# Kernel optimization log

Hardware: AMD Instinct MI355X
Metric: run time of the kernel (lower is better)

The kernel has to match this reference:

```python
import jax, jax.numpy as jnp
import numpy as np

T, B, H, NH = 1024, 4, 1024, 16
D = H // NH


def setup_inputs() -> dict:
    key = jax.random.key(0)
    ks = jax.random.split(key, 8)
    s = 0.02
    return {
        "x": jax.random.normal(ks[0], (T, B, H), jnp.float32),
        "pos": jax.random.normal(ks[1], (2 * T - 1, 1, H), jnp.float32),
        "attn_mask": jnp.zeros((T, T), jnp.bool_),
        "ln_w": jnp.ones((H,), jnp.float32),
        "ln_b": jnp.zeros((H,), jnp.float32),
        "in_proj_w": jax.random.normal(ks[2], (3 * H, H), jnp.float32) * s,
        "in_proj_b": jnp.zeros((3 * H,), jnp.float32),
        "pos_proj_w": jax.random.normal(ks[3], (H, H), jnp.float32) * s,
        "r_w_bias": jax.random.normal(ks[4], (NH, D), jnp.float32) * s,
        "r_r_bias": jax.random.normal(ks[5], (NH, D), jnp.float32) * s,
        "out_proj_w": jax.random.normal(ks[6], (H, H), jnp.float32) * s,
        "out_proj_b": jnp.zeros((H,), jnp.float32),
    }


def _layer_norm(x, w, b, eps=1e-5):
    m = jnp.mean(x, axis=-1, keepdims=True)
    v = jnp.var(x, axis=-1, keepdims=True)
    return (x - m) * jax.lax.rsqrt(v + eps) * w + b


def _rel_shift(x):
    # x: [qlen, 2*qlen-1, B, NH] -> Transformer-XL relative shift
    q = x.shape[0]
    zero_pad = jnp.zeros((q, 1) + x.shape[2:], x.dtype)
    xp = jnp.concatenate([zero_pad, x], axis=1)            # [q, 2q, B, NH]
    xp = xp.reshape((x.shape[1] + 1, q) + x.shape[2:])     # [2q, q, B, NH]
    return xp[1:].reshape(x.shape)                         # [q, 2q-1, B, NH]


def reference(x, pos, attn_mask, ln_w, ln_b, in_proj_w, in_proj_b,
              pos_proj_w, r_w_bias, r_r_bias, out_proj_w, out_proj_b):
    # pre-norm
    qn = _layer_norm(x, ln_w, ln_b)                        # [T,B,H]
    # fused qkv projection
    qkv = qn @ in_proj_w.T + in_proj_b                     # [T,B,3H]
    q, k, v = jnp.split(qkv, 3, axis=-1)
    q = q.reshape(T, B, NH, D)
    k = k.reshape(T, B, NH, D)
    v = v.reshape(T, B, NH, D)
    # relative position keys (bias-free projection)
    r = (pos[:, 0] @ pos_proj_w.T).reshape(2 * T - 1, NH, D)
    # content term (AC) and position term (BD), Transformer-XL style
    AC = jnp.einsum('ibnd,jbnd->ijbn', q + r_w_bias, k)    # [T,T,B,NH]
    BD = jnp.einsum('ibnd,jnd->ijbn', q + r_r_bias, r)     # [T,2T-1,B,NH]
    BD = _rel_shift(BD)[:, :T]                             # [T,T,B,NH]
    scale = 1.0 / np.sqrt(D).astype(np.float32)
    score = (AC + BD) * scale
    score = jnp.where(attn_mask[:, :, None, None], -jnp.inf, score)
    p = jax.nn.softmax(score, axis=1)                      # coverage
    out = jnp.einsum('ijbn,jbnd->ibnd', p, v).reshape(T, B, H)
    o = out @ out_proj_w.T + out_proj_b                    # residual dropout = identity (eval)
    return o
```

## Files before the change

### kernel.cpp

```cpp
#include <hip/hip_runtime.h>
#include <hip/hip_bf16.h>
#include <math.h>

#define T_DIM 1024
#define B_DIM 4
#define H_DIM 1024
#define NHEAD 16
#define DHEAD 64
#define NROWS (T_DIM * B_DIM)
#define LPOS  (2 * T_DIM - 1)
#define QS    (3 * H_DIM)

typedef __attribute__((ext_vector_type(8))) short bfrag;
typedef __attribute__((ext_vector_type(4))) short sh4;
typedef __attribute__((ext_vector_type(4))) float facc;

static __device__ __forceinline__ short f2bf(float f) {
    return __builtin_bit_cast(short, __float2bfloat16(f));
}
static __device__ __forceinline__ float bf2f(short s) {
    unsigned u = ((unsigned)(unsigned short)s) << 16;
    return __builtin_bit_cast(float, u);
}

#define GLD16(g, l) __builtin_amdgcn_global_load_lds( \
    (const __attribute__((address_space(1))) void*)(g), \
    (__attribute__((address_space(3))) void*)(l), 16, 0, 0)

__global__ __launch_bounds__(256) void prep_kernel(
    const float* __restrict__ x, const float* __restrict__ lnw,
    const float* __restrict__ lnb, short* __restrict__ qn,
    const float* __restrict__ s0, short* __restrict__ d0, int c0,
    const float* __restrict__ s1, short* __restrict__ d1, int c1,
    const float* __restrict__ s2, short* __restrict__ d2, int c2,
    const float* __restrict__ s3, short* __restrict__ d3, int c3) {
    __shared__ float red0[4], red1[4];
    const int bid = blockIdx.x;
    const int tid = threadIdx.x;
    if (bid < NROWS) {
        const float* xr = x + (size_t)bid * H_DIM;
        short* yr = qn + (size_t)bid * H_DIM;
        float4 v = reinterpret_cast<const float4*>(xr)[tid];
        float s  = v.x + v.y + v.z + v.w;
        float sq = v.x * v.x + v.y * v.y + v.z * v.z + v.w * v.w;
        #pragma unroll
        for (int m = 32; m; m >>= 1) {
            s  += __shfl_xor(s, m);
            sq += __shfl_xor(sq, m);
        }
        int wave = tid >> 6, lane = tid & 63;
        if (lane == 0) { red0[wave] = s; red1[wave] = sq; }
        __syncthreads();
        float tot   = red0[0] + red0[1] + red0[2] + red0[3];
        float totsq = red1[0] + red1[1] + red1[2] + red1[3];
        float mean = tot * (1.0f / H_DIM);
        float var  = totsq * (1.0f / H_DIM) - mean * mean;
        float rstd = rsqrtf(var + 1e-5f);
        float4 wv = reinterpret_cast<const float4*>(lnw)[tid];
        float4 bv = reinterpret_cast<const float4*>(lnb)[tid];
        sh4 o;
        o[0] = f2bf((v.x - mean) * rstd * wv.x + bv.x);
        o[1] = f2bf((v.y - mean) * rstd * wv.y + bv.y);
        o[2] = f2bf((v.z - mean) * rstd * wv.z + bv.z);
        o[3] = f2bf((v.w - mean) * rstd * wv.w + bv.w);
        reinterpret_cast<sh4*>(yr)[tid] = o;
    } else {
        int i = (bid - NROWS) * 256 + tid;
        const float* s; short* d; int off;
        if      (i < c0)                { s = s0; d = d0; off = i; }
        else if (i < c0 + c1)           { s = s1; d = d1; off = i - c0; }
        else if (i < c0 + c1 + c2)      { s = s2; d = d2; off = i - c0 - c1; }
        else if (i < c0 + c1 + c2 + c3) { s = s3; d = d3; off = i - c0 - c1 - c2; }
        else return;
        const float* sp = s + (size_t)off * 8;
        float4 a = *(const float4*)(sp);
        float4 b = *(const float4*)(sp + 4);
        bfrag f;
        f[0] = f2bf(a.x); f[1] = f2bf(a.y); f[2] = f2bf(a.z); f[3] = f2bf(a.w);
        f[4] = f2bf(b.x); f[5] = f2bf(b.y); f[6] = f2bf(b.z); f[7] = f2bf(b.w);
        *(bfrag*)(d + (size_t)off * 8) = f;
    }
}

template<int MODE>
static __device__ __forceinline__ void gemm_body(
    const short* __restrict__ A, const short* __restrict__ B,
    const float* __restrict__ bias, void* __restrict__ Cv,
    int M, int N, int K, int gx, int nblk, int bid,
    short (*As)[64], short (*Bs)[64]) {
    const int tid = threadIdx.x;
    const int w4 = tid >> 6, l = tid & 63;
    const int lc = l & 15, lg = l >> 4;
    const int wr = w4 >> 1, wc = w4 & 1;

    const int cpx = nblk >> 3;
    const int nl = (bid & 7) * cpx + (bid >> 3);
    const int row0 = (nl / gx) * 128, col0 = (nl % gx) * 128;

    const int srow = l >> 3;
    const int schunk = ((l & 7) ^ srow) * 8;
    const int Mm1 = M - 1;

    facc acc[4][4];
    #pragma unroll
    for (int i = 0; i < 4; ++i)
        #pragma unroll
        for (int j = 0; j < 4; ++j) acc[i][j] = (facc){0.f, 0.f, 0.f, 0.f};

    for (int k0 = 0; k0 < K; k0 += 64) {
        #pragma unroll
        for (int p = 0; p < 4; ++p) {
            int rA = p * 32 + w4 * 8 + srow;
            int ga = row0 + rA; if (ga > Mm1) ga = Mm1;
            GLD16(A + (size_t)ga * K + k0 + schunk,
                  (char*)As + p * 4096 + w4 * 1024);
            GLD16(B + (size_t)(col0 + rA) * K + k0 + schunk,
                  (char*)Bs + p * 4096 + w4 * 1024);
        }
        __syncthreads();

        bfrag af[4][2], bfr[4][2];
        #pragma unroll
        for (int fr = 0; fr < 4; ++fr) {
            const int ra = wr * 64 + fr * 16 + lc;
            #pragma unroll
            for (int ks = 0; ks < 2; ++ks)
                af[fr][ks] = *(const bfrag*)&As[ra][(((ks * 4 + lg) ^ (ra & 7)) << 3)];
        }
        #pragma unroll
        for (int fc = 0; fc < 4; ++fc) {
            const int rb = wc * 64 + fc * 16 + lc;
            #pragma unroll
            for (int ks = 0; ks < 2; ++ks)
                bfr[fc][ks] = *(const bfrag*)&Bs[rb][(((ks * 4 + lg) ^ (rb & 7)) << 3)];
        }
        #pragma unroll
        for (int fr = 0; fr < 4; ++fr)
            #pragma unroll
            for (int fc = 0; fc < 4; ++fc)
                #pragma unroll
                for (int ks = 0; ks < 2; ++ks)
                    acc[fr][fc] = __builtin_amdgcn_mfma_f32_16x16x32_bf16(
                        af[fr][ks], bfr[fc][ks], acc[fr][fc], 0, 0, 0);
        __syncthreads();
    }

    #pragma unroll
    for (int fc = 0; fc < 4; ++fc) {
        const int gc = col0 + wc * 64 + fc * 16 + lc;
        const float bv = bias ? bias[gc] : 0.f;
        #pragma unroll
        for (int fr = 0; fr < 4; ++fr) {
            #pragma unroll
            for (int rg = 0; rg < 4; ++rg) {
                const int gr = row0 + wr * 64 + fr * 16 + lg * 4 + rg;
                if (gr < M) {
                    float o = acc[fr][fc][rg] + bv;
                    if constexpr (MODE == 0) ((float*)Cv)[(size_t)gr * N + gc] = o;
                    else                     ((short*)Cv)[(size_t)gr * N + gc] = f2bf(o);
                }
            }
        }
    }
}

__global__ __launch_bounds__(256) void gemm_dual(
    const short* __restrict__ A0, const short* __restrict__ B0,
    const float* __restrict__ bias0, short* __restrict__ C0,
    const short* __restrict__ A1, const short* __restrict__ B1,
    short* __restrict__ C1) {
    __shared__ short As[128][64];
    __shared__ short Bs[128][64];
    const int bid = blockIdx.x;
    if (bid < 768)
        gemm_body<1>(A0, B0, bias0, C0, NROWS, QS, H_DIM, QS / 128, 768, bid, As, Bs);
    else
        gemm_body<1>(A1, B1, nullptr, C1, LPOS, H_DIM, H_DIM, H_DIM / 128, 128, bid - 768, As, Bs);
}

__global__ __launch_bounds__(256) void gemm_f32out(
    const short* __restrict__ A, const short* __restrict__ B,
    const float* __restrict__ bias, float* __restrict__ C) {
    __shared__ short As[128][64];
    __shared__ short Bs[128][64];
    gemm_body<0>(A, B, bias, C, NROWS, H_DIM, H_DIM, H_DIM / 128, 256, blockIdx.x, As, Bs);
}

__global__ __launch_bounds__(256) void vtrans_kernel(const short* __restrict__ qkv,
                                                     short* __restrict__ vT) {
    __shared__ short T[64][72];
    const int tt = blockIdx.x, hh = blockIdx.y, b = blockIdx.z;
    const int tid = threadIdx.x;
    const int w = tid >> 6, lane = tid & 63;

    const int tg = tt * 64 + lane;
    const short* src = qkv + (size_t)(tg * B_DIM + b) * QS + 2 * H_DIM + hh * 64 + w * 16;
    bfrag v0 = *(const bfrag*)(src);
    bfrag v1 = *(const bfrag*)(src + 8);
    #pragma unroll
    for (int e = 0; e < 8; ++e) T[w * 16 + e][lane] = v0[e];
    #pragma unroll
    for (int e = 0; e < 8; ++e) T[w * 16 + 8 + e][lane] = v1[e];
    __syncthreads();

    const int hd = tid >> 2, tc = tid & 3;
    bfrag o0 = *(const bfrag*)&T[hd][tc * 16];
    bfrag o1 = *(const bfrag*)&T[hd][tc * 16 + 8];
    short* dst = vT + (((size_t)(b * H_DIM + hh * 64 + hd)) << 10) + tt * 64 + tc * 16;
    *(bfrag*)(dst) = o0;
    *(bfrag*)(dst + 8) = o1;
}

__global__ __launch_bounds__(256) void attn_mfma(const short* __restrict__ qkv,
                                                 const short* __restrict__ r,
                                                 const short* __restrict__ vt,
                                                 const float* __restrict__ rwb,
                                                 const float* __restrict__ rrb,
                                                 short* __restrict__ out) {
    __shared__ short Ks[64][64];
    __shared__ short Vt[64][64];
    __shared__ short Rs[128][64];
    __shared__ short BDs[4][16][84];
    __shared__ short Ps[4][16][76];

    const int d_   = blockIdx.y * 16 + blockIdx.x;
    const int slot = d_ >> 3, xcd = d_ & 7;
    const int bn   = xcd + 8 * (slot >> 4);
    const int i0   = (slot & 15) * 64;
    const int b    = bn >> 4;
    const int n    = bn & 15;

    const int tid = threadIdx.x;
    const int w   = tid >> 6;
    const int l   = tid & 63;
    const int lg  = l >> 4;
    const int lc  = l & 15;
    const int hoff = n * DHEAD;

    const int srow8 = l >> 3;
    const int sc8   = ((l & 7) ^ srow8) * 8;

    bfrag qw[2], qr[2];
    {
        const int row = i0 + 16 * w + lc;
        const short* qrow = qkv + (size_t)(row * B_DIM + b) * QS + hoff;
        #pragma unroll
        for (int ks = 0; ks < 2; ++ks) {
            const int d0 = ks * 32 + lg * 8;
            bfrag qv = *(const bfrag*)(qrow + d0);
            float4 wa = *(const float4*)(rwb + hoff + d0);
            float4 wb = *(const float4*)(rwb + hoff + d0 + 4);
            float4 ra = *(const float4*)(rrb + hoff + d0);
            float4 rb = *(const float4*)(rrb + hoff + d0 + 4);
            const float sc = 0.125f * 1.44269504f;
            float wf[8] = {wa.x, wa.y, wa.z, wa.w, wb.x, wb.y, wb.z, wb.w};
            float rf[8] = {ra.x, ra.y, ra.z, ra.w, rb.x, rb.y, rb.z, rb.w};
            bfrag fw, fr;
            #pragma unroll
            for (int e = 0; e < 8; ++e) {
                float qf = bf2f(qv[e]);
                fw[e] = f2bf((qf + wf[e]) * sc);
                fr[e] = f2bf((qf + rf[e]) * sc);
            }
            qw[ks] = fw; qr[ks] = fr;
        }
    }

    facc ofr[4];
    #pragma unroll
    for (int d = 0; d < 4; ++d) ofr[d] = (facc){0.f, 0.f, 0.f, 0.f};
    float lrow[4] = {0.f, 0.f, 0.f, 0.f};
    const int wbase = 16 * (3 - w);

    const short* kp0 = qkv + ((size_t)((w * 2 + 0) * 8 + srow8) * B_DIM + b) * QS + H_DIM + hoff + sc8;
    const short* kp1 = qkv + ((size_t)((w * 2 + 1) * 8 + srow8) * B_DIM + b) * QS + H_DIM + hoff + sc8;
    const short* vp0 = vt + (((size_t)(b * H_DIM + hoff + (w * 2 + 0) * 8 + srow8)) << 10) + sc8;
    const short* vp1 = vt + (((size_t)(b * H_DIM + hoff + (w * 2 + 1) * 8 + srow8)) << 10) + sc8;
    const size_t kstep = (size_t)64 * B_DIM * QS;
    char* const ksd0 = (char*)Ks + (w * 2 + 0) * 1024;
    char* const ksd1 = (char*)Ks + (w * 2 + 1) * 1024;
    char* const vtd0 = (char*)Vt + (w * 2 + 0) * 1024;
    char* const vtd1 = (char*)Vt + (w * 2 + 1) * 1024;

    for (int jt = 0; jt < 16; ++jt) {
        const int l_min = jt * 64 + 960 - i0;

        GLD16(kp0, ksd0);
        GLD16(kp1, ksd1);
        #pragma unroll
        for (int p = 0; p < 4; ++p) {
            const int c16 = w * 4 + p;
            int lrw = l_min + c16 * 8 + srow8; if (lrw > 2046) lrw = 2046;
            GLD16(r + (size_t)lrw * H_DIM + hoff + sc8,
                  (char*)Rs + c16 * 1024);
        }
        GLD16(vp0, vtd0);
        GLD16(vp1, vtd1);
        kp0 += kstep; kp1 += kstep; vp0 += 64; vp1 += 64;
        __syncthreads();

        __builtin_amdgcn_s_setprio(1);
        facc sfr[4];
        #pragma unroll
        for (int js = 0; js < 4; ++js) {
            sfr[js] = (facc){-4.f, -4.f, -4.f, -4.f};
            const int jrow = js * 16 + lc;
            #pragma unroll
            for (int ks = 0; ks < 2; ++ks) {
                const int ch = (ks * 4 + lg) ^ (jrow & 7);
                bfrag bf = *(const bfrag*)&Ks[jrow][ch << 3];
                sfr[js] = __builtin_amdgcn_mfma_f32_16x16x32_bf16(qw[ks], bf, sfr[js], 0, 0, 0);
            }
        }
        #pragma unroll
        for (int ls = 0; ls < 5; ++ls) {
            facc bd = (facc){-4.f, -4.f, -4.f, -4.f};
            const int rrow = wbase + ls * 16 + lc;
            #pragma unroll
            for (int ks = 0; ks < 2; ++ks) {
                const int ch = (ks * 4 + lg) ^ (rrow & 7);
                bfrag bf = *(const bfrag*)&Rs[rrow][ch << 3];
                bd = __builtin_amdgcn_mfma_f32_16x16x32_bf16(qr[ks], bf, bd, 0, 0, 0);
            }
            #pragma unroll
            for (int rg = 0; rg < 4; ++rg)
                BDs[w][lg * 4 + rg][ls * 16 + lc] = f2bf(bd[rg]);
        }
        __builtin_amdgcn_s_setprio(0);

        #pragma unroll
        for (int js = 0; js < 4; ++js)
            #pragma unroll
            for (int rg = 0; rg < 4; ++rg) {
                const int irow = lg * 4 + rg;
                float v = sfr[js][rg] + bf2f(BDs[w][irow][js * 16 + lc - irow + 15]);
                float p = exp2f(v);
                lrow[rg] += p;
                Ps[w][irow][js * 16 + lc] = f2bf(p);
            }

        bfrag pf[2];
        #pragma unroll
        for (int ks = 0; ks < 2; ++ks)
            pf[ks] = *(const bfrag*)&Ps[w][lc][ks * 32 + lg * 8];
        __builtin_amdgcn_s_setprio(1);
        #pragma unroll
        for (int d = 0; d < 4; ++d) {
            #pragma unroll
            for (int ks = 0; ks < 2; ++ks) {
                const int vr = d * 16 + lc;
                const int ch = (ks * 4 + lg) ^ (vr & 7);
                bfrag vf = *(const bfrag*)&Vt[vr][ch << 3];
                ofr[d] = __builtin_amdgcn_mfma_f32_16x16x32_bf16(pf[ks], vf, ofr[d], 0, 0, 0);
            }
        }
        __builtin_amdgcn_s_setprio(0);
        __syncthreads();
    }

    #pragma unroll
    for (int m = 1; m < 16; m <<= 1)
        #pragma unroll
        for (int rg = 0; rg < 4; ++rg)
            lrow[rg] += __shfl_xor(lrow[rg], m);

    #pragma unroll
    for (int rg = 0; rg < 4; ++rg) {
        const float inv = 1.0f / lrow[rg];
        const int row = i0 + 16 * w + lg * 4 + rg;
        short* orow = out + (size_t)(row * B_DIM + b) * H_DIM + hoff;
        #pragma unroll
        for (int d = 0; d < 4; ++d)
            orow[d * 16 + lc] = f2bf(ofr[d][rg] * inv);
    }
}

extern "C" void kernel_launch(void* const* d_in, const int* in_sizes, int n_in,
                              void* d_out, int out_size, void* d_ws, size_t ws_size,
                              hipStream_t stream) {
    const float* x          = (const float*)d_in[0];
    const float* pos        = (const float*)d_in[1];
    const float* ln_w       = (const float*)d_in[3];
    const float* ln_b       = (const float*)d_in[4];
    const float* in_proj_w  = (const float*)d_in[5];
    const float* in_proj_b  = (const float*)d_in[6];
    const float* pos_proj_w = (const float*)d_in[7];
    const float* r_w_bias   = (const float*)d_in[8];
    const float* r_r_bias   = (const float*)d_in[9];
    const float* out_proj_w = (const float*)d_in[10];
    const float* out_proj_b = (const float*)d_in[11];
    float* out = (float*)d_out;

    short* qn   = (short*)d_ws;
    short* qkv  = qn + (size_t)NROWS * H_DIM;
    short* rbuf = qkv + (size_t)NROWS * QS;
    short* wi   = rbuf + (size_t)2048 * H_DIM;
    short* wp   = wi + (size_t)QS * H_DIM;
    short* wo   = wp + (size_t)H_DIM * H_DIM;
    short* posb = wo + (size_t)H_DIM * H_DIM;
    short* vT   = posb + (size_t)2048 * H_DIM;

    const int c0 = (LPOS * H_DIM) / 8;
    const int c1 = (QS * H_DIM) / 8;
    const int c2 = (H_DIM * H_DIM) / 8;
    const int c3 = c2;
    const int nchunk = c0 + c1 + c2 + c3;
    const int cvtblk = (nchunk + 255) / 256;
    prep_kernel<<<NROWS + cvtblk, 256, 0, stream>>>(
        x, ln_w, ln_b, qn,
        pos, posb, c0, in_proj_w, wi, c1, pos_proj_w, wp, c2, out_proj_w, wo, c3);

    gemm_dual<<<768 + 128, 256, 0, stream>>>(qn, wi, in_proj_b, qkv, posb, wp, rbuf);

    vtrans_kernel<<<dim3(16, 16, 4), 256, 0, stream>>>(qkv, vT);

    attn_mfma<<<dim3(T_DIM / 64, B_DIM * NHEAD), 256, 0, stream>>>(
        qkv, rbuf, vT, r_w_bias, r_r_bias, qn);

    gemm_f32out<<<256, 256, 0, stream>>>(qn, wo, out_proj_b, out);
}
```

Baseline: 184.2 us.

## Prefetch next K/V/R tiles into registers to overlap global loads with compute

Replaces the direct global-to-LDS loads at the top of each key-tile iteration with register staging. The next tile's K, V and R fragments are loaded into registers while the current tile's MFMAs run, then written to LDS after a barrier. The goal is to hide global memory latency behind the score and PV computation. In exchange it costs extra VGPRs for the staging buffers and adds a second barrier per iteration, which may hurt occupancy.

New measurement: 175.5 us. 4.7% less time.

```diff
diff --git a/kernel.cpp b/kernel.cpp
--- a/kernel.cpp
+++ b/kernel.cpp
@@ -277,27 +277,40 @@
     const short* vp0 = vt + (((size_t)(b * H_DIM + hoff + (w * 2 + 0) * 8 + srow8)) << 10) + sc8;
     const short* vp1 = vt + (((size_t)(b * H_DIM + hoff + (w * 2 + 1) * 8 + srow8)) << 10) + sc8;
     const size_t kstep = (size_t)64 * B_DIM * QS;
-    char* const ksd0 = (char*)Ks + (w * 2 + 0) * 1024;
-    char* const ksd1 = (char*)Ks + (w * 2 + 1) * 1024;
-    char* const vtd0 = (char*)Vt + (w * 2 + 0) * 1024;
-    char* const vtd1 = (char*)Vt + (w * 2 + 1) * 1024;
-
-    for (int jt = 0; jt < 16; ++jt) {
+    bfrag* const ksd0 = (bfrag*)((char*)Ks + (w * 2 + 0) * 1024 + l * 16);
+    bfrag* const ksd1 = (bfrag*)((char*)Ks + (w * 2 + 1) * 1024 + l * 16);
+    bfrag* const vtd0 = (bfrag*)((char*)Vt + (w * 2 + 0) * 1024 + l * 16);
+    bfrag* const vtd1 = (bfrag*)((char*)Vt + (w * 2 + 1) * 1024 + l * 16);
+
+    bfrag stK0, stK1, stV0, stV1, stR[4];
+
+    auto load_regs = [&](int jt) {
         const int l_min = jt * 64 + 960 - i0;
-
-        GLD16(kp0, ksd0);
-        GLD16(kp1, ksd1);
+        stK0 = *(const bfrag*)(kp0 + (size_t)jt * kstep);
+        stK1 = *(const bfrag*)(kp1 + (size_t)jt * kstep);
+        stV0 = *(const bfrag*)(vp0 + jt * 64);
+        stV1 = *(const bfrag*)(vp1 + jt * 64);
         #pragma unroll
         for (int p = 0; p < 4; ++p) {
             const int c16 = w * 4 + p;
             int lrw = l_min + c16 * 8 + srow8; if (lrw > 2046) lrw = 2046;
-            GLD16(r + (size_t)lrw * H_DIM + hoff + sc8,
-                  (char*)Rs + c16 * 1024);
-        }
-        GLD16(vp0, vtd0);
-        GLD16(vp1, vtd1);
-        kp0 += kstep; kp1 += kstep; vp0 += 64; vp1 += 64;
-        __syncthreads();
+            stR[p] = *(const bfrag*)(r + (size_t)lrw * H_DIM + hoff + sc8);
+        }
+    };
+    auto write_lds = [&]() {
+        *ksd0 = stK0; *ksd1 = stK1;
+        *vtd0 = stV0; *vtd1 = stV1;
+        #pragma unroll
+        for (int p = 0; p < 4; ++p)
+            *(bfrag*)((char*)Rs + (w * 4 + p) * 1024 + l * 16) = stR[p];
+    };
+
+    load_regs(0);
+    write_lds();
+    __syncthreads();
+
+    for (int jt = 0; jt < 16; ++jt) {
+        if (jt < 15) load_regs(jt + 1);
 
         __builtin_amdgcn_s_setprio(1);
         facc sfr[4];
@@ -355,7 +368,12 @@
             }
         }
         __builtin_amdgcn_s_setprio(0);
+
         __syncthreads();
+        if (jt < 15) {
+            write_lds();
+            __syncthreads();
+        }
     }
 
     #pragma unroll
```
